# Performance work log

Measured on AMD Instinct MI355X. Metric: run time of the kernel, lower is better.

Reference implementation:

```python
import jax, jax.numpy as jnp
import numpy as np

EPS = 1e-5
NUM_HEADS = 2
SR = 4

def layer_norm(x, g, b):
    m = jnp.mean(x, axis=-1, keepdims=True)
    v = jnp.mean((x - m) ** 2, axis=-1, keepdims=True)
    return (x - m) * jax.lax.rsqrt(v + EPS) * g + b

def grid_idx(loc_orig, H, W):
    # loc_orig in [-1,1] -> nearest pixel index in HxW grid
    loc = (jnp.clip(loc_orig, -1.0, 1.0) + 1.0) * 0.5
    xi = jnp.round(loc[..., 0] * (W - 1)).astype(jnp.int32)
    yi = jnp.round(loc[..., 1] * (H - 1)).astype(jnp.int32)
    return yi * W + xi  # [B, N0]

def token2map(tok, loc_orig, idx_agg, H, W):
    # scatter token features to an HxW map, averaging over orig locations per cell
    B, N, C = tok.shape
    idx_hw = grid_idx(loc_orig, H, W)
    feat = jnp.take_along_axis(tok, idx_agg[..., None], axis=1)  # [B,N0,C]
    def scat(f, idx):
        num = jax.ops.segment_sum(f, idx, num_segments=H * W)
        cnt = jax.ops.segment_sum(jnp.ones(f.shape[:1], f.dtype), idx, num_segments=H * W)
        return num / jnp.maximum(cnt, 1.0)[:, None]
    return jax.vmap(scat)(feat, idx_hw).reshape(B, H, W, C)

def map2token(x_map, N, loc_orig, idx_agg, agg_weight):
    # nearest-sample map at orig locations, weighted-average per token
    B, H, W, C = x_map.shape
    idx_hw = grid_idx(loc_orig, H, W)
    val = jnp.take_along_axis(x_map.reshape(B, H * W, C), idx_hw[..., None], axis=1)  # [B,N0,C]
    def agg(v, w, idx):
        num = jax.ops.segment_sum(v * w, idx, num_segments=N)
        den = jax.ops.segment_sum(w, idx, num_segments=N)
        return num / jnp.maximum(den, 1e-6)
    return jax.vmap(agg)(val, agg_weight, idx_agg)

def block_fwd(x, loc_orig, idx_agg, agg_weight, x_source, idx_agg_source, conf_source,
              ln1_g, ln1_b, ln2_g, ln2_b, wq, wkv, wproj, bproj, sr_w, sr_b,
              srn_g, srn_b, fc1_w, fc1_b, dw_w, dw_b, dwskip_w, fc2_w, fc2_b, H, W):
    B, N, C = x.shape
    d = C // NUM_HEADS
    scale = d ** -0.5
    # ---- attention (MyAttention, sr_ratio>1 path) ----
    xn = layer_norm(x, ln1_g, ln1_b)
    xsn = layer_norm(x_source, ln1_g, ln1_b)
    q = (xn @ wq).reshape(B, N, NUM_HEADS, d).transpose(0, 2, 1, 3)  # [B,h,N,d]
    tmp = jnp.concatenate([xsn, conf_source], axis=-1)  # [B,Ns,C+1]
    tmap = token2map(tmp, loc_orig, idx_agg_source, H, W)  # [B,H,W,C+1]
    xs_map, conf_map = tmap[..., :C], tmap[..., C:]
    xs = jax.lax.conv_general_dilated(xs_map, sr_w, (SR, SR), 'VALID',
                                      dimension_numbers=('NHWC', 'HWIO', 'NHWC')) + sr_b
    h2, w2 = xs.shape[1], xs.shape[2]
    xs = layer_norm(xs.reshape(B, h2 * w2, C), srn_g, srn_b)  # [B,M,C]
    conf_p = conf_map.reshape(B, h2, SR, w2, SR).mean(axis=(2, 4)).reshape(B, h2 * w2)
    kv = (xs @ wkv).reshape(B, h2 * w2, 2, NUM_HEADS, d)
    k = kv[:, :, 0].transpose(0, 2, 1, 3)  # [B,h,M,d]
    v = kv[:, :, 1].transpose(0, 2, 1, 3)
    attn = jnp.einsum('bhnd,bhmd->bhnm', q, k) * scale + conf_p[:, None, None, :]
    attn = jax.nn.softmax(attn, axis=-1)
    out = jnp.einsum('bhnm,bhmd->bhnd', attn, v).transpose(0, 2, 1, 3).reshape(B, N, C)
    x1 = x + (out @ wproj + bproj)
    # ---- MLP (MyMlp with MyDWConv) ----
    y = layer_norm(x1, ln2_g, ln2_b)
    h = y @ fc1_w + fc1_b  # [B,N,hid]
    hid = h.shape[-1]
    hmap = token2map(h, loc_orig, idx_agg, H, W)  # [B,H,W,hid]
    hmap = jax.lax.conv_general_dilated(hmap, dw_w, (1, 1), 'SAME',
                                        dimension_numbers=('NHWC', 'HWIO', 'NHWC'),
                                        feature_group_count=hid) + dw_b
    ht = map2token(hmap, N, loc_orig, idx_agg, agg_weight) + h * dwskip_w
    ht = jax.nn.gelu(ht, approximate=False)
    return x1 + (ht @ fc2_w + fc2_b)

def setup_inputs() -> dict:
    key = jax.random.key(0)
    ks = jax.random.split(key, 20)
    B, N, N0, Ns, C, H, W = 8, 4096, 16384, 16384, 128, 64, 64
    hid = 4 * C
    def rn(k, shape, std=0.02):
        return jax.random.normal(k, shape, dtype=jnp.float32) * std
    return {
        'x': jax.random.normal(ks[0], (B, N, C), jnp.float32),
        'loc_orig': jax.random.uniform(ks[1], (B, N0, 2), jnp.float32, -1.0, 1.0),
        'idx_agg': jax.random.randint(ks[2], (B, N0), 0, N),
        'agg_weight': jax.random.uniform(ks[3], (B, N0, 1), jnp.float32),
        'x_source': jax.random.normal(ks[4], (B, Ns, C), jnp.float32),
        'idx_agg_source': jax.random.randint(ks[5], (B, N0), 0, Ns),
        'conf_source': jax.random.normal(ks[6], (B, Ns, 1), jnp.float32) * 0.1,
        'ln1_g': jnp.ones((C,), jnp.float32), 'ln1_b': jnp.zeros((C,), jnp.float32),
        'ln2_g': jnp.ones((C,), jnp.float32), 'ln2_b': jnp.zeros((C,), jnp.float32),
        'wq': rn(ks[7], (C, C)), 'wkv': rn(ks[8], (C, 2 * C)),
        'wproj': rn(ks[9], (C, C)), 'bproj': jnp.zeros((C,), jnp.float32),
        'sr_w': rn(ks[10], (4, 4, C, C)), 'sr_b': jnp.zeros((C,), jnp.float32),
        'srn_g': jnp.ones((C,), jnp.float32), 'srn_b': jnp.zeros((C,), jnp.float32),
        'fc1_w': rn(ks[11], (C, hid)), 'fc1_b': jnp.zeros((hid,), jnp.float32),
        'dw_w': rn(ks[12], (3, 3, 1, hid), 0.1), 'dw_b': jnp.zeros((hid,), jnp.float32),
        'dwskip_w': rn(ks[13], (hid,), 0.1) + 1.0,
        'fc2_w': rn(ks[14], (hid, C)), 'fc2_b': jnp.zeros((C,), jnp.float32),
        'H': H, 'W': W,
    }

def reference(x, loc_orig, idx_agg, agg_weight, x_source, idx_agg_source, conf_source,
              ln1_g, ln1_b, ln2_g, ln2_b, wq, wkv, wproj, bproj, sr_w, sr_b,
              srn_g, srn_b, fc1_w, fc1_b, dw_w, dw_b, dwskip_w, fc2_w, fc2_b, H, W):
    return block_fwd(x, loc_orig, idx_agg, agg_weight, x_source, idx_agg_source, conf_source,
                     ln1_g, ln1_b, ln2_g, ln2_b, wq, wkv, wproj, bproj, sr_w, sr_b,
                     srn_g, srn_b, fc1_w, fc1_b, dw_w, dw_b, dwskip_w, fc2_w, fc2_b, H, W)
```

## Files before the change

### kernel.cpp

```cpp
#include <hip/hip_runtime.h>

typedef unsigned short u16;
typedef unsigned int   u32;
typedef short bf16x8 __attribute__((ext_vector_type(8)));
typedef float f32x4  __attribute__((ext_vector_type(4)));

#define MFMA16(a,b,c) __builtin_amdgcn_mfma_f32_16x16x32_bf16((a),(b),(c),0,0,0)

__device__ __forceinline__ float bf2f(u32 u){ union{u32 i; float f;} v; v.i = u<<16; return v.f; }
__device__ __forceinline__ u16 f2bf(float f){
  union{float f; u32 i;} v; v.f=f; u32 i=v.i;
  return (u16)((i + 0x7fffu + ((i>>16)&1u)) >> 16);
}
__device__ __forceinline__ u32 pk2(float a, float b){ return (u32)f2bf(a) | ((u32)f2bf(b)<<16); }
__device__ __forceinline__ float geluf(float x){ return 0.5f*x*(1.f + erff(x*0.7071067811865475f)); }

__global__ void k_prep(const float* __restrict__ wq, u16* __restrict__ wqT,
                       const float* __restrict__ wkv, u16* __restrict__ wkvT,
                       const float* __restrict__ wproj, u16* __restrict__ wprojT,
                       const float* __restrict__ fc1w, u16* __restrict__ fc1T,
                       const float* __restrict__ fc2w, u16* __restrict__ fc2T,
                       const float* __restrict__ srw, u16* __restrict__ srwT,
                       const float* __restrict__ loc, const int* __restrict__ iagg,
                       int* __restrict__ idx_hw, int* __restrict__ cnt_all){
  int t = blockIdx.x*256 + threadIdx.x;
  if(t < 458752){
    const float* w; u16* wt; int li, Nsh, K;
    if(t < 16384){ w=wq; wt=wqT; li=t; Nsh=7; K=128; }
    else if(t < 49152){ w=wkv; wt=wkvT; li=t-16384; Nsh=8; K=128; }
    else if(t < 65536){ w=wproj; wt=wprojT; li=t-49152; Nsh=7; K=128; }
    else if(t < 131072){ w=fc1w; wt=fc1T; li=t-65536; Nsh=9; K=128; }
    else if(t < 196608){ w=fc2w; wt=fc2T; li=t-131072; Nsh=7; K=512; }
    else { w=srw; wt=srwT; li=t-196608; Nsh=7; K=2048; }
    int k = li >> Nsh, n = li & ((1<<Nsh)-1);
    wt[(size_t)n*K + k] = f2bf(w[li]);
  } else {
    int tid = t - 458752;
    int b = tid >> 14;
    float lx = loc[(size_t)tid*2];
    float ly = loc[(size_t)tid*2+1];
    float tx = (fminf(fmaxf(lx,-1.f),1.f)+1.f)*0.5f;
    float ty = (fminf(fmaxf(ly,-1.f),1.f)+1.f)*0.5f;
    int xi = (int)rintf(tx*63.f);
    int yi = (int)rintf(ty*63.f);
    int cell = yi*64 + xi;
    idx_hw[tid] = cell;
    atomicAdd(&cnt_all[b*4096 + cell], 1);
    atomicAdd(&cnt_all[(8+b)*4096 + iagg[tid]], 1);
  }
}

__device__ __forceinline__ void ln_row_quarter(const float* __restrict__ in, u16* __restrict__ outp,
    const float* __restrict__ g, const float* __restrict__ bt, int part){
  const float4* src = (const float4*)(in + part*32);
  float4 v[8];
  #pragma unroll
  for(int j=0;j<8;j++) v[j] = src[j];
  float s = 0.f, ss = 0.f;
  #pragma unroll
  for(int j=0;j<8;j++){
    s  += v[j].x + v[j].y + v[j].z + v[j].w;
    ss += v[j].x*v[j].x + v[j].y*v[j].y + v[j].z*v[j].z + v[j].w*v[j].w;
  }
  s  += __shfl_xor(s,1,64);  ss += __shfl_xor(ss,1,64);
  s  += __shfl_xor(s,2,64);  ss += __shfl_xor(ss,2,64);
  float mean = s*(1.f/128.f);
  float rstd = rsqrtf(ss*(1.f/128.f) - mean*mean + 1e-5f);
  const float4* gp = (const float4*)(g + part*32);
  const float4* bp = (const float4*)(bt + part*32);
  u32 o[16];
  #pragma unroll
  for(int j=0;j<8;j++){
    float4 gg = gp[j], bb = bp[j];
    o[2*j]   = pk2((v[j].x-mean)*rstd*gg.x + bb.x, (v[j].y-mean)*rstd*gg.y + bb.y);
    o[2*j+1] = pk2((v[j].z-mean)*rstd*gg.z + bb.z, (v[j].w-mean)*rstd*gg.w + bb.w);
  }
  int4* dst = (int4*)(outp + part*32);
  #pragma unroll
  for(int j=0;j<4;j++) dst[j] = ((const int4*)o)[j];
}

__global__ __launch_bounds__(256) void k_ln_x2(const float* __restrict__ in0, u16* __restrict__ out0,
    const float* __restrict__ in1, u16* __restrict__ out1,
    const float* __restrict__ g, const float* __restrict__ bt){
  int t = blockIdx.x*256 + threadIdx.x;
  int row = t >> 2, part = t & 3;
  const float* in; u16* outp;
  if(row < 32768){ in = in0 + (size_t)row*128; outp = out0 + (size_t)row*128; }
  else { int r2 = row - 32768; in = in1 + (size_t)r2*128; outp = out1 + (size_t)r2*128; }
  ln_row_quarter(in, outp, g, bt, part);
}

__global__ __launch_bounds__(256) void k_ln_f(const float* __restrict__ in, u16* __restrict__ outp,
    const float* __restrict__ g, const float* __restrict__ bt, int rows){
  int t = blockIdx.x*256 + threadIdx.x;
  int row = t >> 2, part = t & 3;
  if(row >= rows) return;
  ln_row_quarter(in + (size_t)row*128, outp + (size_t)row*128, g, bt, part);
}

__global__ __launch_bounds__(256) void k_ln_sr(const float* __restrict__ part, const float* __restrict__ srb,
    const float* __restrict__ g, const float* __restrict__ bt, u16* __restrict__ outp){
  int t = blockIdx.x*256 + threadIdx.x;
  int row = t >> 2, pq = t & 3;
  const float4* p0 = (const float4*)(part +            (size_t)row*128 + pq*32);
  const float4* p1 = (const float4*)(part + 262144  +  (size_t)row*128 + pq*32);
  const float4* p2 = (const float4*)(part + 524288  +  (size_t)row*128 + pq*32);
  const float4* p3 = (const float4*)(part + 786432  +  (size_t)row*128 + pq*32);
  const float4* sb = (const float4*)(srb + pq*32);
  float4 v[8];
  float s = 0.f, ss = 0.f;
  #pragma unroll
  for(int j=0;j<8;j++){
    float4 a = p0[j], b2 = p1[j], c = p2[j], d = p3[j], e = sb[j];
    v[j].x = a.x+b2.x+c.x+d.x+e.x;
    v[j].y = a.y+b2.y+c.y+d.y+e.y;
    v[j].z = a.z+b2.z+c.z+d.z+e.z;
    v[j].w = a.w+b2.w+c.w+d.w+e.w;
    s  += v[j].x + v[j].y + v[j].z + v[j].w;
    ss += v[j].x*v[j].x + v[j].y*v[j].y + v[j].z*v[j].z + v[j].w*v[j].w;
  }
  s  += __shfl_xor(s,1,64);  ss += __shfl_xor(ss,1,64);
  s  += __shfl_xor(s,2,64);  ss += __shfl_xor(ss,2,64);
  float mean = s*(1.f/128.f);
  float rstd = rsqrtf(ss*(1.f/128.f) - mean*mean + 1e-5f);
  const float4* gp = (const float4*)(g + pq*32);
  const float4* bp = (const float4*)(bt + pq*32);
  u32 o[16];
  #pragma unroll
  for(int j=0;j<8;j++){
    float4 gg = gp[j], bb = bp[j];
    o[2*j]   = pk2((v[j].x-mean)*rstd*gg.x + bb.x, (v[j].y-mean)*rstd*gg.y + bb.y);
    o[2*j+1] = pk2((v[j].z-mean)*rstd*gg.z + bb.z, (v[j].w-mean)*rstd*gg.w + bb.w);
  }
  int4* dst = (int4*)(outp + (size_t)row*128 + pq*32);
  #pragma unroll
  for(int j=0;j<4;j++) dst[j] = ((const int4*)o)[j];
}

__global__ __launch_bounds__(1024) void k_scan(const int* __restrict__ cnt_all,
    int* __restrict__ offs_all, int* __restrict__ cur_all){
  int g = blockIdx.x;
  const int* src = cnt_all + g*4096;
  int* offs = offs_all + g*4097;
  int* cur  = cur_all  + g*4096;
  __shared__ int part[1024];
  int t = threadIdx.x;
  int v0=src[4*t], v1=src[4*t+1], v2=src[4*t+2], v3=src[4*t+3];
  int s = v0+v1+v2+v3;
  part[t] = s; __syncthreads();
  for(int off=1; off<1024; off<<=1){
    int x = (t>=off) ? part[t-off] : 0;
    __syncthreads();
    part[t] += x;
    __syncthreads();
  }
  int base = part[t] - s;
  offs[4*t]   = base;          cur[4*t]   = base;
  offs[4*t+1] = base+v0;       cur[4*t+1] = base+v0;
  offs[4*t+2] = base+v0+v1;    cur[4*t+2] = base+v0+v1;
  offs[4*t+3] = base+v0+v1+v2; cur[4*t+3] = base+v0+v1+v2;
  if(t==1023) offs[4096] = base+s;
}

__global__ void k_fill(const int* __restrict__ idx_hw, const int* __restrict__ iagg,
                       int* __restrict__ cur_all, int* __restrict__ list_all){
  int tid = blockIdx.x*256 + threadIdx.x;
  int b = tid >> 14, i = tid & 16383;
  int cell = idx_hw[tid];
  int p = atomicAdd(&cur_all[b*4096 + cell], 1);
  list_all[(b<<14) + p] = i;
  int tok = iagg[tid];
  p = atomicAdd(&cur_all[(8+b)*4096 + tok], 1);
  list_all[((8+b)<<14) + p] = i;
}

__global__ __launch_bounds__(64) void k_tmap(const u16* __restrict__ xsn, const float* __restrict__ confs,
    const int* __restrict__ iaggs, const int* __restrict__ offs_all, const int* __restrict__ list_all,
    u16* __restrict__ xs_map, float* __restrict__ conf_p){
  int b = blockIdx.x >> 12, cell = blockIdx.x & 4095;
  int lane = threadIdx.x;
  int st = offs_all[b*4097 + cell], en = offs_all[b*4097 + cell + 1];
  float a0=0.f, a1=0.f, cf=0.f;
  for(int p=st;p<en;p+=4){
    int idx[4]; float vm[4];
    #pragma unroll
    for(int j=0;j<4;j++){
      int pj = (p+j < en) ? p+j : en-1;
      vm[j] = (p+j < en) ? 1.f : 0.f;
      idx[j] = list_all[(b<<14)+pj];
    }
    int src[4];
    #pragma unroll
    for(int j=0;j<4;j++) src[j] = iaggs[(b<<14)+idx[j]];
    u32 u[4]; float cfv[4];
    #pragma unroll
    for(int j=0;j<4;j++){
      u[j]   = ((const u32*)(xsn + ((size_t)(b<<14)+src[j])*128))[lane];
      cfv[j] = confs[(b<<14)+src[j]];
    }
    #pragma unroll
    for(int j=0;j<4;j++){
      a0 += vm[j]*bf2f(u[j] & 0xffffu);
      a1 += vm[j]*bf2f(u[j] >> 16);
      cf += vm[j]*cfv[j];
    }
  }
  float inv = 1.f/fmaxf((float)(en-st), 1.f);
  ((u32*)(xs_map + ((size_t)(b<<12)+cell)*128))[lane] = pk2(a0*inv, a1*inv);
  if(lane==0){
    int ci = ((cell>>8)<<4) + ((cell&63)>>2);
    atomicAdd(&conf_p[b*256 + ci], cf*inv*(1.f/16.f));
  }
}

__global__ __launch_bounds__(256) void k_gemm_sr(const u16* __restrict__ xs_map, const u16* __restrict__ Wt,
    float* __restrict__ part){
  __shared__ __attribute__((aligned(16))) u16 lA[128*80];
  __shared__ __attribute__((aligned(16))) u16 lB[128*80];
  int m0 = blockIdx.x*128;
  int kbase = blockIdx.y*512;
  int tid = threadIdx.x, lane = tid & 63, wv = tid >> 6;
  int wm = (wv>>1)*64, wn = (wv&1)*64;
  int l16 = lane & 15, q4 = lane >> 4;
  f32x4 acc[4][4];
  for(int i=0;i<4;i++) for(int j=0;j<4;j++) acc[i][j] = (f32x4){0.f,0.f,0.f,0.f};
  for(int k0=kbase; k0<kbase+512; k0+=64){
    __syncthreads();
    for(int s=0;s<4;s++){
      int c = tid + s*256;
      int row = c >> 3, ko = (c & 7)*8;
      int m = m0 + row, k = k0 + ko;
      int b = m >> 8, oc = m & 255;
      int oy = oc >> 4, ox = oc & 15;
      int pos = k >> 7, ch = k & 127;
      int r = pos >> 2, ssp = pos & 3;
      int gy = oy*4 + r, gx = ox*4 + ssp;
      *(int4*)(lA + row*80 + ko) =
          *(const int4*)(xs_map + ((size_t)(b*4096) + gy*64 + gx)*128 + ch);
      *(int4*)(lB + row*80 + ko) = *(const int4*)(Wt + (size_t)row*2048 + k);
    }
    __syncthreads();
    for(int kk=0;kk<64;kk+=32){
      bf16x8 af[4], bfr[4];
      for(int i=0;i<4;i++) af[i]  = *(const bf16x8*)(lA + (wm + i*16 + l16)*80 + kk + q4*8);
      for(int j=0;j<4;j++) bfr[j] = *(const bf16x8*)(lB + (wn + j*16 + l16)*80 + kk + q4*8);
      for(int i=0;i<4;i++)
        for(int j=0;j<4;j++)
          acc[i][j] = MFMA16(af[i], bfr[j], acc[i][j]);
    }
  }
  float* outp = part + (size_t)blockIdx.y*262144;
  for(int i=0;i<4;i++) for(int j=0;j<4;j++){
    int col = wn + j*16 + l16;
    for(int r=0;r<4;r++){
      int row = m0 + wm + i*16 + q4*4 + r;
      outp[(size_t)row*128 + col] = acc[i][j][r];
    }
  }
}

__global__ __launch_bounds__(256) void k_gemm(const u16* __restrict__ Ag, const u16* __restrict__ Wt,
    const float* __restrict__ bias, const float* __restrict__ resf,
    u16* __restrict__ outb, float* __restrict__ outf, int M, int N, int K){
  __shared__ __attribute__((aligned(16))) u16 lA[128*80];
  __shared__ __attribute__((aligned(16))) u16 lB[128*80];
  int m0 = blockIdx.x*128, n0 = blockIdx.y*128;
  int tid = threadIdx.x, lane = tid & 63, wv = tid >> 6;
  int wm = (wv>>1)*64, wn = (wv&1)*64;
  int l16 = lane & 15, q4 = lane >> 4;
  f32x4 acc[4][4];
  for(int i=0;i<4;i++) for(int j=0;j<4;j++) acc[i][j] = (f32x4){0.f,0.f,0.f,0.f};
  for(int k0=0;k0<K;k0+=64){
    __syncthreads();
    for(int s=0;s<4;s++){
      int c = tid + s*256;
      int row = c >> 3, ko = (c & 7)*8;
      *(int4*)(lA + row*80 + ko) = *(const int4*)(Ag + (size_t)(m0+row)*K + k0 + ko);
      *(int4*)(lB + row*80 + ko) = *(const int4*)(Wt + (size_t)(n0+row)*K + k0 + ko);
    }
    __syncthreads();
    for(int kk=0;kk<64;kk+=32){
      bf16x8 af[4], bfr[4];
      for(int i=0;i<4;i++) af[i]  = *(const bf16x8*)(lA + (wm + i*16 + l16)*80 + kk + q4*8);
      for(int j=0;j<4;j++) bfr[j] = *(const bf16x8*)(lB + (wn + j*16 + l16)*80 + kk + q4*8);
      for(int i=0;i<4;i++)
        for(int j=0;j<4;j++)
          acc[i][j] = MFMA16(af[i], bfr[j], acc[i][j]);
    }
  }
  for(int i=0;i<4;i++) for(int j=0;j<4;j++){
    int col = n0 + wn + j*16 + l16;
    float bv = bias ? bias[col] : 0.f;
    for(int r=0;r<4;r++){
      int row = m0 + wm + i*16 + q4*4 + r;
      size_t oo = (size_t)row*N + col;
      float v = acc[i][j][r] + bv;
      if(resf) v += resf[oo];
      if(outf) outf[oo] = v;
      else     outb[oo] = f2bf(v);
    }
  }
}

__global__ void k_vtrans(const u16* __restrict__ kvout, u16* __restrict__ vtg){
  int t = blockIdx.x*256 + threadIdx.x;
  int n = t & 255, dd = (t>>8) & 63, bh = t >> 14;
  int b = bh >> 1, h = bh & 1;
  vtg[t] = kvout[((size_t)(b*256 + n))*256 + 128 + h*64 + dd];
}

__global__ __launch_bounds__(256) void k_attn(const u16* __restrict__ qb, const u16* __restrict__ kvb,
    const u16* __restrict__ vtg, const float* __restrict__ confp, u16* __restrict__ o){
  __shared__ __attribute__((aligned(16))) u16 Pl[4*16*264];
  __shared__ float cl[256];
  int bh = blockIdx.x >> 5, qblk = blockIdx.x & 31;
  int b = bh >> 1, h = bh & 1;
  int tid = threadIdx.x, lane = tid & 63, wv = tid >> 6;
  cl[tid] = confp[b*256 + tid];
  __syncthreads();
  int l16 = lane & 15, q4 = lane >> 4;
  u16* P = Pl + wv*(16*264);
  for(int it=0; it<2; it++){
    int q0 = qblk*128 + wv*32 + it*16;
    const u16* qrow = qb + ((size_t)(b*4096) + q0 + l16)*128 + h*64 + q4*8;
    bf16x8 aq0 = *(const bf16x8*)(qrow);
    bf16x8 aq1 = *(const bf16x8*)(qrow + 32);
    f32x4 sAcc[16];
    for(int nt=0; nt<16; nt++){
      const u16* krow = kvb + ((size_t)(b*256) + nt*16 + l16)*256 + h*64 + q4*8;
      bf16x8 bk0 = *(const bf16x8*)(krow);
      bf16x8 bk1 = *(const bf16x8*)(krow + 32);
      f32x4 z = (f32x4){0.f,0.f,0.f,0.f};
      z = MFMA16(aq0, bk0, z);
      z = MFMA16(aq1, bk1, z);
      sAcc[nt] = z;
    }
    float rmax[4] = {-3e38f,-3e38f,-3e38f,-3e38f};
    for(int nt=0;nt<16;nt++){
      float cb = cl[nt*16 + l16];
      for(int r=0;r<4;r++){
        float s = sAcc[nt][r]*0.125f + cb;
        sAcc[nt][r] = s;
        rmax[r] = fmaxf(rmax[r], s);
      }
    }
    for(int m=1;m<16;m<<=1)
      for(int r=0;r<4;r++) rmax[r] = fmaxf(rmax[r], __shfl_xor(rmax[r], m, 64));
    float rsum[4] = {0.f,0.f,0.f,0.f};
    for(int nt=0;nt<16;nt++)
      for(int r=0;r<4;r++){ float p = __expf(sAcc[nt][r]-rmax[r]); sAcc[nt][r]=p; rsum[r]+=p; }
    for(int m=1;m<16;m<<=1)
      for(int r=0;r<4;r++) rsum[r] += __shfl_xor(rsum[r], m, 64);
    for(int nt=0;nt<16;nt++)
      for(int r=0;r<4;r++) P[(q4*4+r)*264 + nt*16 + l16] = f2bf(sAcc[nt][r]);
    __syncthreads();
    f32x4 oAcc[4];
    for(int dt=0;dt<4;dt++) oAcc[dt] = (f32x4){0.f,0.f,0.f,0.f};
    for(int kc=0;kc<8;kc++){
      bf16x8 ap = *(const bf16x8*)(P + l16*264 + kc*32 + q4*8);
      for(int dt=0; dt<4; dt++){
        const u16* vrow = vtg + ((size_t)(bh*64) + dt*16 + l16)*256 + kc*32 + q4*8;
        bf16x8 bv = *(const bf16x8*)(vrow);
        oAcc[dt] = MFMA16(ap, bv, oAcc[dt]);
      }
    }
    float rinv[4]; for(int r=0;r<4;r++) rinv[r] = 1.f/rsum[r];
    for(int dt=0;dt<4;dt++)
      for(int r=0;r<4;r++){
        int row = q0 + q4*4 + r, col = h*64 + dt*16 + l16;
        o[((size_t)(b*4096)+row)*128 + col] = f2bf(oAcc[dt][r]*rinv[r]);
      }
    __syncthreads();
  }
}

__global__ __launch_bounds__(128) void k_hmap(const u16* __restrict__ hsrc, const int* __restrict__ iagg,
    const int* __restrict__ offs_all, const int* __restrict__ list_all, u16* __restrict__ hmap){
  int b = blockIdx.x >> 12, cell = blockIdx.x & 4095;
  int c0 = threadIdx.x*4;
  int st = offs_all[b*4097+cell], en = offs_all[b*4097+cell+1];
  float a0=0.f,a1=0.f,a2=0.f,a3=0.f;
  for(int p=st;p<en;p+=4){
    int idx[4]; float vm[4];
    #pragma unroll
    for(int j=0;j<4;j++){
      int pj = (p+j < en) ? p+j : en-1;
      vm[j] = (p+j < en) ? 1.f : 0.f;
      idx[j] = list_all[(b<<14)+pj];
    }
    int src[4];
    #pragma unroll
    for(int j=0;j<4;j++) src[j] = iagg[(b<<14)+idx[j]];
    uint2 u[4];
    #pragma unroll
    for(int j=0;j<4;j++) u[j] = *(const uint2*)(hsrc + ((size_t)(b<<12)+src[j])*512 + c0);
    #pragma unroll
    for(int j=0;j<4;j++){
      a0 += vm[j]*bf2f(u[j].x & 0xffffu); a1 += vm[j]*bf2f(u[j].x >> 16);
      a2 += vm[j]*bf2f(u[j].y & 0xffffu); a3 += vm[j]*bf2f(u[j].y >> 16);
    }
  }
  float inv = 1.f/fmaxf((float)(en-st), 1.f);
  uint2 o; o.x = pk2(a0*inv, a1*inv); o.y = pk2(a2*inv, a3*inv);
  *(uint2*)(hmap + ((size_t)(b<<12)+cell)*512 + c0) = o;
}

__global__ __launch_bounds__(256) void k_dw(const u16* __restrict__ hmap, const float* __restrict__ dww,
    const float* __restrict__ dwb, u16* __restrict__ outm){
  int g = blockIdx.x*256 + threadIdx.x;
  int cq = g & 127;
  int xg = (g>>7) & 15;
  int yy = (g>>11) & 63;
  int b  = g >> 17;
  int c0 = cq*4;
  int x0 = xg*4;
  float4 bb = *(const float4*)(dwb + c0);
  float acc[4][4];
  for(int xo=0;xo<4;xo++){ acc[xo][0]=bb.x; acc[xo][1]=bb.y; acc[xo][2]=bb.z; acc[xo][3]=bb.w; }
  for(int r=0;r<3;r++){
    int ys = yy + r - 1;
    if(ys < 0 || ys > 63) continue;
    const u16* rp = hmap + ((size_t)((b<<12) + ys*64))*512;
    float col[6][4];
    for(int cc=0;cc<6;cc++){
      int xx = x0 + cc - 1;
      uint2 u = make_uint2(0u,0u);
      if(xx >= 0 && xx <= 63) u = *(const uint2*)(rp + (size_t)xx*512 + c0);
      col[cc][0]=bf2f(u.x&0xffffu); col[cc][1]=bf2f(u.x>>16);
      col[cc][2]=bf2f(u.y&0xffffu); col[cc][3]=bf2f(u.y>>16);
    }
    for(int s=0;s<3;s++){
      float4 wv = *(const float4*)(dww + (r*3+s)*512 + c0);
      for(int xo=0;xo<4;xo++){
        acc[xo][0] += wv.x*col[xo+s][0];
        acc[xo][1] += wv.y*col[xo+s][1];
        acc[xo][2] += wv.z*col[xo+s][2];
        acc[xo][3] += wv.w*col[xo+s][3];
      }
    }
  }
  for(int xo=0;xo<4;xo++){
    int pos = (b<<12) + yy*64 + x0 + xo;
    uint2 o; o.x = pk2(acc[xo][0],acc[xo][1]); o.y = pk2(acc[xo][2],acc[xo][3]);
    *(uint2*)(outm + (size_t)pos*512 + c0) = o;
  }
}

__global__ __launch_bounds__(128) void k_m2t(const u16* __restrict__ hdw, const u16* __restrict__ hbuf,
    const float* __restrict__ aggw, const int* __restrict__ idx_hw, const int* __restrict__ offs_all,
    const int* __restrict__ list_all, const float* __restrict__ dwskip, u16* __restrict__ ht){
  int b = blockIdx.x >> 12, tok = blockIdx.x & 4095;
  int c0 = threadIdx.x*4;
  int st = offs_all[(8+b)*4097+tok], en = offs_all[(8+b)*4097+tok+1];
  float n0=0.f,n1=0.f,n2=0.f,n3=0.f,den=0.f;
  for(int p=st;p<en;p+=4){
    int idx[4]; float vm[4];
    #pragma unroll
    for(int j=0;j<4;j++){
      int pj = (p+j < en) ? p+j : en-1;
      vm[j] = (p+j < en) ? 1.f : 0.f;
      idx[j] = list_all[((8+b)<<14)+pj];
    }
    float w[4]; int cell[4];
    #pragma unroll
    for(int j=0;j<4;j++){
      w[j] = vm[j]*aggw[(b<<14)+idx[j]];
      cell[j] = idx_hw[(b<<14)+idx[j]];
    }
    uint2 u[4];
    #pragma unroll
    for(int j=0;j<4;j++) u[j] = *(const uint2*)(hdw + ((size_t)(b<<12)+cell[j])*512 + c0);
    #pragma unroll
    for(int j=0;j<4;j++){
      n0 += w[j]*bf2f(u[j].x & 0xffffu); n1 += w[j]*bf2f(u[j].x >> 16);
      n2 += w[j]*bf2f(u[j].y & 0xffffu); n3 += w[j]*bf2f(u[j].y >> 16);
      den += w[j];
    }
  }
  float inv = 1.f/fmaxf(den, 1e-6f);
  uint2 hu = *(const uint2*)(hbuf + ((size_t)(b<<12)+tok)*512 + c0);
  float4 sk = *(const float4*)(dwskip + c0);
  float v0 = geluf(n0*inv + bf2f(hu.x&0xffffu)*sk.x);
  float v1 = geluf(n1*inv + bf2f(hu.x>>16)   *sk.y);
  float v2 = geluf(n2*inv + bf2f(hu.y&0xffffu)*sk.z);
  float v3 = geluf(n3*inv + bf2f(hu.y>>16)   *sk.w);
  uint2 o; o.x=pk2(v0,v1); o.y=pk2(v2,v3);
  *(uint2*)(ht + ((size_t)(b<<12)+tok)*512 + c0) = o;
}

extern "C" void kernel_launch(void* const* d_in, const int* in_sizes, int n_in,
                              void* d_out, int out_size, void* d_ws, size_t ws_size,
                              hipStream_t stream){
  (void)in_sizes; (void)n_in; (void)out_size; (void)ws_size;
  const float* x     = (const float*)d_in[0];
  const float* loc   = (const float*)d_in[1];
  const int*   iagg  = (const int*)d_in[2];
  const float* aggw  = (const float*)d_in[3];
  const float* xsrc  = (const float*)d_in[4];
  const int*   iaggs = (const int*)d_in[5];
  const float* confs = (const float*)d_in[6];
  const float* ln1g  = (const float*)d_in[7];
  const float* ln1b  = (const float*)d_in[8];
  const float* ln2g  = (const float*)d_in[9];
  const float* ln2b  = (const float*)d_in[10];
  const float* wq    = (const float*)d_in[11];
  const float* wkv   = (const float*)d_in[12];
  const float* wproj = (const float*)d_in[13];
  const float* bproj = (const float*)d_in[14];
  const float* srw   = (const float*)d_in[15];
  const float* srb   = (const float*)d_in[16];
  const float* srng  = (const float*)d_in[17];
  const float* srnb  = (const float*)d_in[18];
  const float* fc1w  = (const float*)d_in[19];
  const float* fc1b  = (const float*)d_in[20];
  const float* dww   = (const float*)d_in[21];
  const float* dwb   = (const float*)d_in[22];
  const float* dwskip= (const float*)d_in[23];
  const float* fc2w  = (const float*)d_in[24];
  const float* fc2b  = (const float*)d_in[25];
  float* out = (float*)d_out;

  char* ws = (char*)d_ws;
  size_t off = 0;
  auto A = [&](size_t n)->char*{ char* p = ws + off; off = (off + n + 255) & ~(size_t)255; return p; };
  int*   cnt_all  = (int*)A(16*4096*4);
  float* conf_p   = (float*)A(8*256*4);
  int*   offs_all = (int*)A(16*4097*4);
  int*   cur_all  = (int*)A(16*4096*4);
  int*   list_all = (int*)A(16*16384*4);
  int*   idx_hw   = (int*)A(8*16384*4);
  u16* wqT    = (u16*)A(128*128*2);
  u16* wkvT   = (u16*)A(256*128*2);
  u16* wprojT = (u16*)A(128*128*2);
  u16* fc1T   = (u16*)A(512*128*2);
  u16* fc2T   = (u16*)A(128*512*2);
  u16* srwT   = (u16*)A(128*2048*2);
  char* R0 = A(33554432);
  char* R1 = A(33554432);
  char* R2 = A(33554432);
  char* R3 = A(8388608);
  char* R4 = A(16777216);
  u16* xsn    = (u16*)R0;  u16* hbuf = (u16*)R0;
  u16* hmap   = (u16*)R1;  u16* ht   = (u16*)R1;
  u16* xn     = (u16*)R2;
  u16* attn_o = (u16*)R2;
  u16* qout   = (u16*)(R2 + 8388608);
  float* xs_part = (float*)(R2 + 16777216);
  u16* kvout  = (u16*)(R2 + 25165824);
  u16* vtg    = (u16*)(R2 + 26214400);
  u16* xs     = (u16*)(R2 + 27262976);
  u16* hdw    = (u16*)R2;
  u16* xs_map = (u16*)R3;  u16* ybuf = (u16*)R3;
  float* x1   = (float*)R4;

  hipMemsetAsync(cnt_all, 0, 16*4096*4 + 8*256*4, stream);

  k_prep<<<dim3(2304), 256, 0, stream>>>(wq, wqT, wkv, wkvT, wproj, wprojT,
      fc1w, fc1T, fc2w, fc2T, srw, srwT, loc, iagg, idx_hw, cnt_all);

  k_ln_x2<<<dim3(2560), 256, 0, stream>>>(x, xn, xsrc, xsn, ln1g, ln1b);

  k_scan<<<dim3(16), 1024, 0, stream>>>(cnt_all, offs_all, cur_all);
  k_fill<<<dim3(512), 256, 0, stream>>>(idx_hw, iagg, cur_all, list_all);

  k_tmap<<<dim3(32768), 64, 0, stream>>>(xsn, confs, iaggs, offs_all, list_all, xs_map, conf_p);

  k_gemm_sr<<<dim3(16,4), 256, 0, stream>>>(xs_map, srwT, xs_part);
  k_ln_sr<<<dim3(32), 256, 0, stream>>>(xs_part, srb, srng, srnb, xs);

  k_gemm<<<dim3(256,1), 256, 0, stream>>>(xn, wqT, nullptr, nullptr, qout, nullptr, 32768, 128, 128);
  k_gemm<<<dim3(16,2),  256, 0, stream>>>(xs, wkvT, nullptr, nullptr, kvout, nullptr, 2048, 256, 128);
  k_vtrans<<<dim3(1024), 256, 0, stream>>>(kvout, vtg);

  k_attn<<<dim3(512), 256, 0, stream>>>(qout, kvout, vtg, conf_p, attn_o);

  k_gemm<<<dim3(256,1), 256, 0, stream>>>(attn_o, wprojT, bproj, x, nullptr, x1, 32768, 128, 128);
  k_ln_f<<<dim3(512), 256, 0, stream>>>(x1, ybuf, ln2g, ln2b, 32768);
  k_gemm<<<dim3(256,4), 256, 0, stream>>>(ybuf, fc1T, fc1b, nullptr, hbuf, nullptr, 32768, 512, 128);

  k_hmap<<<dim3(32768), 128, 0, stream>>>(hbuf, iagg, offs_all, list_all, hmap);
  k_dw<<<dim3(4096), 256, 0, stream>>>(hmap, dww, dwb, hdw);
  k_m2t<<<dim3(32768), 128, 0, stream>>>(hdw, hbuf, aggw, idx_hw, offs_all, list_all, dwskip, ht);

  k_gemm<<<dim3(256,1), 256, 0, stream>>>(ht, fc2T, fc2b, x1, nullptr, out, 32768, 128, 512);
}
```

Before: 483.2 us.

## Fuse LayerNorm into Q and FC1 GEMM prologues; widen LN thread mapping

Adds a GEMM kernel that loads fp32 rows, applies LayerNorm and converts to bf16 directly into shared memory, replacing the separate LN kernels before the Q projection and FC1. This removes the bf16 intermediate write and read for 32768x128 rows. For FC1 the LN is recomputed by each of the 4 column-block groups. The remaining LN kernels now use 32 threads per row with one float4 each instead of 4 threads per row, for more parallelism and better-coalesced loads.

New measurement: 443.2 us. 8.3% less time.

```diff
diff --git a/kernel.cpp b/kernel.cpp
--- a/kernel.cpp
+++ b/kernel.cpp
@@ -50,92 +50,52 @@
   }
 }
 
-__device__ __forceinline__ void ln_row_quarter(const float* __restrict__ in, u16* __restrict__ outp,
-    const float* __restrict__ g, const float* __restrict__ bt, int part){
-  const float4* src = (const float4*)(in + part*32);
-  float4 v[8];
+__global__ __launch_bounds__(256) void k_ln1(const float* __restrict__ in, u16* __restrict__ outp,
+    const float* __restrict__ g, const float* __restrict__ bt){
+  int t = blockIdx.x*256 + threadIdx.x;
+  int row = t >> 5, c = t & 31;
+  float4 v = ((const float4*)(in + (size_t)row*128))[c];
+  float s  = v.x + v.y + v.z + v.w;
+  float ss = v.x*v.x + v.y*v.y + v.z*v.z + v.w*v.w;
   #pragma unroll
-  for(int j=0;j<8;j++) v[j] = src[j];
-  float s = 0.f, ss = 0.f;
-  #pragma unroll
-  for(int j=0;j<8;j++){
-    s  += v[j].x + v[j].y + v[j].z + v[j].w;
-    ss += v[j].x*v[j].x + v[j].y*v[j].y + v[j].z*v[j].z + v[j].w*v[j].w;
-  }
-  s  += __shfl_xor(s,1,64);  ss += __shfl_xor(ss,1,64);
-  s  += __shfl_xor(s,2,64);  ss += __shfl_xor(ss,2,64);
+  for(int m=1;m<32;m<<=1){ s += __shfl_xor(s,m,64); ss += __shfl_xor(ss,m,64); }
   float mean = s*(1.f/128.f);
   float rstd = rsqrtf(ss*(1.f/128.f) - mean*mean + 1e-5f);
-  const float4* gp = (const float4*)(g + part*32);
-  const float4* bp = (const float4*)(bt + part*32);
-  u32 o[16];
-  #pragma unroll
-  for(int j=0;j<8;j++){
-    float4 gg = gp[j], bb = bp[j];
-    o[2*j]   = pk2((v[j].x-mean)*rstd*gg.x + bb.x, (v[j].y-mean)*rstd*gg.y + bb.y);
-    o[2*j+1] = pk2((v[j].z-mean)*rstd*gg.z + bb.z, (v[j].w-mean)*rstd*gg.w + bb.w);
-  }
-  int4* dst = (int4*)(outp + part*32);
-  #pragma unroll
-  for(int j=0;j<4;j++) dst[j] = ((const int4*)o)[j];
-}
-
-__global__ __launch_bounds__(256) void k_ln_x2(const float* __restrict__ in0, u16* __restrict__ out0,
-    const float* __restrict__ in1, u16* __restrict__ out1,
-    const float* __restrict__ g, const float* __restrict__ bt){
-  int t = blockIdx.x*256 + threadIdx.x;
-  int row = t >> 2, part = t & 3;
-  const float* in; u16* outp;
-  if(row < 32768){ in = in0 + (size_t)row*128; outp = out0 + (size_t)row*128; }
-  else { int r2 = row - 32768; in = in1 + (size_t)r2*128; outp = out1 + (size_t)r2*128; }
-  ln_row_quarter(in, outp, g, bt, part);
-}
-
-__global__ __launch_bounds__(256) void k_ln_f(const float* __restrict__ in, u16* __restrict__ outp,
-    const float* __restrict__ g, const float* __restrict__ bt, int rows){
-  int t = blockIdx.x*256 + threadIdx.x;
-  int row = t >> 2, part = t & 3;
-  if(row >= rows) return;
-  ln_row_quarter(in + (size_t)row*128, outp + (size_t)row*128, g, bt, part);
+  float4 gg = ((const float4*)g)[c];
+  float4 bb = ((const float4*)bt)[c];
+  uint2 o;
+  o.x = pk2((v.x-mean)*rstd*gg.x + bb.x, (v.y-mean)*rstd*gg.y + bb.y);
+  o.y = pk2((v.z-mean)*rstd*gg.z + bb.z, (v.w-mean)*rstd*gg.w + bb.w);
+  ((uint2*)(outp + (size_t)row*128))[c] = o;
 }
 
 __global__ __launch_bounds__(256) void k_ln_sr(const float* __restrict__ part, const float* __restrict__ srb,
     const float* __restrict__ g, const float* __restrict__ bt, u16* __restrict__ outp){
   int t = blockIdx.x*256 + threadIdx.x;
-  int row = t >> 2, pq = t & 3;
-  const float4* p0 = (const float4*)(part +            (size_t)row*128 + pq*32);
-  const float4* p1 = (const float4*)(part + 262144  +  (size_t)row*128 + pq*32);
-  const float4* p2 = (const float4*)(part + 524288  +  (size_t)row*128 + pq*32);
-  const float4* p3 = (const float4*)(part + 786432  +  (size_t)row*128 + pq*32);
-  const float4* sb = (const float4*)(srb + pq*32);
-  float4 v[8];
-  float s = 0.f, ss = 0.f;
+  int row = t >> 5, c = t & 31;
+  const float4* p0 = (const float4*)(part +           (size_t)row*128);
+  const float4* p1 = (const float4*)(part + 262144 +  (size_t)row*128);
+  const float4* p2 = (const float4*)(part + 524288 +  (size_t)row*128);
+  const float4* p3 = (const float4*)(part + 786432 +  (size_t)row*128);
+  float4 a = p0[c], b2 = p1[c], cc = p2[c], d = p3[c];
+  float4 e = ((const float4*)srb)[c];
+  float4 v;
+  v.x = a.x+b2.x+cc.x+d.x+e.x;
+  v.y = a.y+b2.y+cc.y+d.y+e.y;
+  v.z = a.z+b2.z+cc.z+d.z+e.z;
+  v.w = a.w+b2.w+cc.w+d.w+e.w;
+  float s  = v.x + v.y + v.z + v.w;
+  float ss = v.x*v.x + v.y*v.y + v.z*v.z + v.w*v.w;
   #pragma unroll
-  for(int j=0;j<8;j++){
-    float4 a = p0[j], b2 = p1[j], c = p2[j], d = p3[j], e = sb[j];
-    v[j].x = a.x+b2.x+c.x+d.x+e.x;
-    v[j].y = a.y+b2.y+c.y+d.y+e.y;
-    v[j].z = a.z+b2.z+c.z+d.z+e.z;
-    v[j].w = a.w+b2.w+c.w+d.w+e.w;
-    s  += v[j].x + v[j].y + v[j].z + v[j].w;
-    ss += v[j].x*v[j].x + v[j].y*v[j].y + v[j].z*v[j].z + v[j].w*v[j].w;
-  }
-  s  += __shfl_xor(s,1,64);  ss += __shfl_xor(ss,1,64);
-  s  += __shfl_xor(s,2,64);  ss += __shfl_xor(ss,2,64);
+  for(int m=1;m<32;m<<=1){ s += __shfl_xor(s,m,64); ss += __shfl_xor(ss,m,64); }
   float mean = s*(1.f/128.f);
   float rstd = rsqrtf(ss*(1.f/128.f) - mean*mean + 1e-5f);
-  const float4* gp = (const float4*)(g + pq*32);
-  const float4* bp = (const float4*)(bt + pq*32);
-  u32 o[16];
-  #pragma unroll
-  for(int j=0;j<8;j++){
-    float4 gg = gp[j], bb = bp[j];
-    o[2*j]   = pk2((v[j].x-mean)*rstd*gg.x + bb.x, (v[j].y-mean)*rstd*gg.y + bb.y);
-    o[2*j+1] = pk2((v[j].z-mean)*rstd*gg.z + bb.z, (v[j].w-mean)*rstd*gg.w + bb.w);
-  }
-  int4* dst = (int4*)(outp + (size_t)row*128 + pq*32);
-  #pragma unroll
-  for(int j=0;j<4;j++) dst[j] = ((const int4*)o)[j];
+  float4 gg = ((const float4*)g)[c];
+  float4 bb = ((const float4*)bt)[c];
+  uint2 o;
+  o.x = pk2((v.x-mean)*rstd*gg.x + bb.x, (v.y-mean)*rstd*gg.y + bb.y);
+  o.y = pk2((v.z-mean)*rstd*gg.z + bb.z, (v.w-mean)*rstd*gg.w + bb.w);
+  ((uint2*)(outp + (size_t)row*128))[c] = o;
 }
 
 __global__ __launch_bounds__(1024) void k_scan(const int* __restrict__ cnt_all,
@@ -299,6 +259,77 @@
       if(resf) v += resf[oo];
       if(outf) outf[oo] = v;
       else     outb[oo] = f2bf(v);
+    }
+  }
+}
+
+__global__ __launch_bounds__(256) void k_gemm_ln(const float* __restrict__ Af,
+    const float* __restrict__ g, const float* __restrict__ bt,
+    const u16* __restrict__ Wt, const float* __restrict__ bias,
+    u16* __restrict__ outb, int N){
+  __shared__ __attribute__((aligned(16))) u16 lA[128*136];
+  __shared__ __attribute__((aligned(16))) u16 lB[128*136];
+  int m0 = blockIdx.x*128, n0 = blockIdx.y*128;
+  int tid = threadIdx.x, lane = tid & 63, wv = tid >> 6;
+  int wm = (wv>>1)*64, wn = (wv&1)*64;
+  int l16 = lane & 15, q4 = lane >> 4;
+  {
+    int p = tid & 7;
+    const float4* gp = (const float4*)(g + p*16);
+    const float4* bp = (const float4*)(bt + p*16);
+    float4 gv[4], bv[4];
+    #pragma unroll
+    for(int j=0;j<4;j++){ gv[j] = gp[j]; bv[j] = bp[j]; }
+    for(int grp=0; grp<4; grp++){
+      int row = grp*32 + (tid>>3);
+      const float4* src = (const float4*)(Af + (size_t)(m0+row)*128 + p*16);
+      float4 v[4];
+      #pragma unroll
+      for(int j=0;j<4;j++) v[j] = src[j];
+      float s = 0.f, ss = 0.f;
+      #pragma unroll
+      for(int j=0;j<4;j++){
+        s  += v[j].x + v[j].y + v[j].z + v[j].w;
+        ss += v[j].x*v[j].x + v[j].y*v[j].y + v[j].z*v[j].z + v[j].w*v[j].w;
+      }
+      s += __shfl_xor(s,1,64); ss += __shfl_xor(ss,1,64);
+      s += __shfl_xor(s,2,64); ss += __shfl_xor(ss,2,64);
+      s += __shfl_xor(s,4,64); ss += __shfl_xor(ss,4,64);
+      float mean = s*(1.f/128.f);
+      float rstd = rsqrtf(ss*(1.f/128.f) - mean*mean + 1e-5f);
+      u32 o[8];
+      #pragma unroll
+      for(int j=0;j<4;j++){
+        o[2*j]   = pk2((v[j].x-mean)*rstd*gv[j].x + bv[j].x, (v[j].y-mean)*rstd*gv[j].y + bv[j].y);
+        o[2*j+1] = pk2((v[j].z-mean)*rstd*gv[j].z + bv[j].z, (v[j].w-mean)*rstd*gv[j].w + bv[j].w);
+      }
+      int4* dst = (int4*)(lA + row*136 + p*16);
+      dst[0] = ((const int4*)o)[0];
+      dst[1] = ((const int4*)o)[1];
+    }
+  }
+  for(int s2=0;s2<8;s2++){
+    int c = tid + s2*256;
+    int row = c >> 4, ko = (c & 15)*8;
+    *(int4*)(lB + row*136 + ko) = *(const int4*)(Wt + (size_t)(n0+row)*128 + ko);
+  }
+  __syncthreads();
+  f32x4 acc[4][4];
+  for(int i=0;i<4;i++) for(int j=0;j<4;j++) acc[i][j] = (f32x4){0.f,0.f,0.f,0.f};
+  for(int kk=0;kk<128;kk+=32){
+    bf16x8 af[4], bfr[4];
+    for(int i=0;i<4;i++) af[i]  = *(const bf16x8*)(lA + (wm + i*16 + l16)*136 + kk + q4*8);
+    for(int j=0;j<4;j++) bfr[j] = *(const bf16x8*)(lB + (wn + j*16 + l16)*136 + kk + q4*8);
+    for(int i=0;i<4;i++)
+      for(int j=0;j<4;j++)
+        acc[i][j] = MFMA16(af[i], bfr[j], acc[i][j]);
+  }
+  for(int i=0;i<4;i++) for(int j=0;j<4;j++){
+    int col = n0 + wn + j*16 + l16;
+    float bv = bias ? bias[col] : 0.f;
+    for(int r=0;r<4;r++){
+      int row = m0 + wm + i*16 + q4*4 + r;
+      outb[(size_t)row*N + col] = f2bf(acc[i][j][r] + bv);
     }
   }
 }
@@ -543,7 +574,6 @@
   char* R4 = A(16777216);
   u16* xsn    = (u16*)R0;  u16* hbuf = (u16*)R0;
   u16* hmap   = (u16*)R1;  u16* ht   = (u16*)R1;
-  u16* xn     = (u16*)R2;
   u16* attn_o = (u16*)R2;
   u16* qout   = (u16*)(R2 + 8388608);
   float* xs_part = (float*)(R2 + 16777216);
@@ -551,7 +581,7 @@
   u16* vtg    = (u16*)(R2 + 26214400);
   u16* xs     = (u16*)(R2 + 27262976);
   u16* hdw    = (u16*)R2;
-  u16* xs_map = (u16*)R3;  u16* ybuf = (u16*)R3;
+  u16* xs_map = (u16*)R3;
   float* x1   = (float*)R4;
 
   hipMemsetAsync(cnt_all, 0, 16*4096*4 + 8*256*4, stream);
@@ -559,7 +589,7 @@
   k_prep<<<dim3(2304), 256, 0, stream>>>(wq, wqT, wkv, wkvT, wproj, wprojT,
       fc1w, fc1T, fc2w, fc2T, srw, srwT, loc, iagg, idx_hw, cnt_all);
 
-  k_ln_x2<<<dim3(2560), 256, 0, stream>>>(x, xn, xsrc, xsn, ln1g, ln1b);
+  k_ln1<<<dim3(16384), 256, 0, stream>>>(xsrc, xsn, ln1g, ln1b);
 
   k_scan<<<dim3(16), 1024, 0, stream>>>(cnt_all, offs_all, cur_all);
   k_fill<<<dim3(512), 256, 0, stream>>>(idx_hw, iagg, cur_all, list_all);
@@ -567,17 +597,16 @@
   k_tmap<<<dim3(32768), 64, 0, stream>>>(xsn, confs, iaggs, offs_all, list_all, xs_map, conf_p);
 
   k_gemm_sr<<<dim3(16,4), 256, 0, stream>>>(xs_map, srwT, xs_part);
-  k_ln_sr<<<dim3(32), 256, 0, stream>>>(xs_part, srb, srng, srnb, xs);
-
-  k_gemm<<<dim3(256,1), 256, 0, stream>>>(xn, wqT, nullptr, nullptr, qout, nullptr, 32768, 128, 128);
+  k_ln_sr<<<dim3(256), 256, 0, stream>>>(xs_part, srb, srng, srnb, xs);
+
+  k_gemm_ln<<<dim3(256,1), 256, 0, stream>>>(x, ln1g, ln1b, wqT, nullptr, qout, 128);
   k_gemm<<<dim3(16,2),  256, 0, stream>>>(xs, wkvT, nullptr, nullptr, kvout, nullptr, 2048, 256, 128);
   k_vtrans<<<dim3(1024), 256, 0, stream>>>(kvout, vtg);
 
   k_attn<<<dim3(512), 256, 0, stream>>>(qout, kvout, vtg, conf_p, attn_o);
 
   k_gemm<<<dim3(256,1), 256, 0, stream>>>(attn_o, wprojT, bproj, x, nullptr, x1, 32768, 128, 128);
-  k_ln_f<<<dim3(512), 256, 0, stream>>>(x1, ybuf, ln2g, ln2b, 32768);
-  k_gemm<<<dim3(256,4), 256, 0, stream>>>(ybuf, fc1T, fc1b, nullptr, hbuf, nullptr, 32768, 512, 128);
+  k_gemm_ln<<<dim3(256,4), 256, 0, stream>>>(x1, ln2g, ln2b, fc1T, fc1b, hbuf, 512);
 
   k_hmap<<<dim3(32768), 128, 0, stream>>>(hbuf, iagg, offs_all, list_all, hmap);
   k_dw<<<dim3(4096), 256, 0, stream>>>(hmap, dww, dwb, hdw);
```
